# Kernel tuning notes

Hardware: AMD Instinct MI355X
Metric: run time of the kernel (lower is better)

The kernel has to match this reference:

```python
import jax, jax.numpy as jnp
import numpy as np

IN_FEATURES = 512
FEATURES = 512
BATCH, SEQ = 8, 8192


def _ste(x_orig, y_proc):
    return x_orig + jax.lax.stop_gradient(y_proc - x_orig)


def setup_inputs() -> dict:
    key = jax.random.key(0)
    kx, kw = jax.random.split(key)
    x = jax.random.normal(kx, (BATCH, SEQ, IN_FEATURES), dtype=jnp.float32)
    # variance_scaling(1.0, 'fan_in', 'normal'): std = 1/sqrt(fan_in)
    weight = jax.random.normal(kw, (IN_FEATURES, FEATURES), dtype=jnp.float32) / np.sqrt(IN_FEATURES)
    bias = jnp.zeros((FEATURES,), dtype=jnp.float32)
    return {"x": x, "weight": weight, "bias": bias}


def reference(x, weight, bias):
    # BitNet 1.58b-style weight binarization with STE
    weight_centered = weight - jnp.mean(weight)
    weight_bin = jnp.sign(weight_centered)
    weight_bin_ste = _ste(weight, weight_bin)
    scale_gamma = jnp.mean(jnp.abs(weight))
    effective_weight = weight_bin_ste * scale_gamma  # [in, out]
    y = jnp.dot(x, effective_weight) + bias  # [B, S, out]
    # NF4-style activation quant-dequant with STE
    act_clipped = jnp.clip(y, -1.0, 1.0)
    quant_dequant = jnp.round(act_clipped * 7.0) / 7.0
    return _ste(y, quant_dequant)
```

## Files before the change

kernel.cpp:

```cpp
#include <hip/hip_runtime.h>
#include <math.h>

#define K_DIM 512
#define N_DIM 512
#define NLEAF 2048
#define BM 128
#define BN 128
#define BK 32

#define WS_LEAFS 16
#define WS_LEAFA (16 + NLEAF)


__global__ void leaf_kernel(const float* __restrict__ w, float* __restrict__ ws) {
  const int leaf = blockIdx.x * blockDim.x + threadIdx.x;
  const float* p = w + leaf * 128;
  float rs[8], ra[8];
  #pragma unroll
  for (int j = 0; j < 8; ++j) { const float v = p[j]; rs[j] = v; ra[j] = fabsf(v); }
  for (int i = 8; i < 128; i += 8) {
    #pragma unroll
    for (int j = 0; j < 8; ++j) { const float v = p[i + j]; rs[j] += v; ra[j] += fabsf(v); }
  }
  ws[WS_LEAFS + leaf] = ((rs[0] + rs[1]) + (rs[2] + rs[3])) + ((rs[4] + rs[5]) + (rs[6] + rs[7]));
  ws[WS_LEAFA + leaf] = ((ra[0] + ra[1]) + (ra[2] + ra[3])) + ((ra[4] + ra[5]) + (ra[6] + ra[7]));
}

__global__ void tree_kernel(float* __restrict__ ws) {
  __shared__ float bufS[4096];
  __shared__ float bufA[4096];
  const int t = threadIdx.x;
  for (int i = t; i < NLEAF; i += 256) {
    bufS[i] = ws[WS_LEAFS + i];
    bufA[i] = ws[WS_LEAFA + i];
  }
  __syncthreads();
  int src = 0, n = NLEAF;
  while (n > 1) {
    const int dst = src + n;
    n >>= 1;
    for (int i = t; i < n; i += 256) {
      bufS[dst + i] = bufS[src + 2 * i] + bufS[src + 2 * i + 1];
      bufA[dst + i] = bufA[src + 2 * i] + bufA[src + 2 * i + 1];
    }
    __syncthreads();
    src = dst;
  }
  if (t == 0) {
    ws[0] = bufS[src] * (1.0f / 262144.0f);
    ws[1] = bufA[src] * (1.0f / 262144.0f);
  }
}

__global__ __launch_bounds__(256, 4) void gemm_kernel(
    const float* __restrict__ x, const float* __restrict__ w,
    const float* __restrict__ bias, const float* __restrict__ ws,
    float* __restrict__ out) {
  __shared__ float As[BM][BK + 4];
  __shared__ float Bs[BK][BN + 4];

  const float mu = ws[0];
  const float gamma = ws[1];
  const int t = threadIdx.x;
  const int tx = t & 15;
  const int ty = t >> 4;
  const int rowBase = blockIdx.x * BM;
  const int colBase = blockIdx.y * BN;

  float acc[2][2][4][4];
  #pragma unroll
  for (int h = 0; h < 2; ++h)
    #pragma unroll
    for (int g = 0; g < 2; ++g)
      #pragma unroll
      for (int i = 0; i < 4; ++i)
        #pragma unroll
        for (int j = 0; j < 4; ++j) acc[h][g][i][j] = 0.0f;

  for (int kc = 0; kc < K_DIM; kc += BK) {
    #pragma unroll
    for (int p = 0; p < 4; ++p) {
      const int r = (t >> 3) + 32 * p;
      const int k4 = (t & 7) * 4;
      const float4 v = *(const float4*)&x[(size_t)(rowBase + r) * K_DIM + kc + k4];
      *(float4*)&As[r][k4] = v;
    }
    #pragma unroll
    for (int p = 0; p < 4; ++p) {
      const int kk = (t >> 5) + 8 * p;
      const int n4 = (t & 31) * 4;
      const float4 v = *(const float4*)&w[(size_t)(kc + kk) * N_DIM + colBase + n4];
      float4 e;
      const float* vi = &v.x;
      float* ei = &e.x;
      #pragma unroll
      for (int c = 0; c < 4; ++c) {
        const float wv = vi[c];
        const float wc = wv - mu;
        const float bin = (wc > 0.0f) ? 1.0f : ((wc < 0.0f) ? -1.0f : 0.0f);
        const float ste = wv + (bin - wv);
        ei[c] = ste * gamma;
      }
      *(float4*)&Bs[kk][n4] = e;
    }
    __syncthreads();

    #pragma unroll
    for (int kg = 0; kg < 8; ++kg) {
      float4 a0[4], a1[4];
      #pragma unroll
      for (int i = 0; i < 4; ++i) {
        a0[i] = *(const float4*)&As[ty * 4 + i][kg * 4];
        a1[i] = *(const float4*)&As[64 + ty * 4 + i][kg * 4];
      }
      #pragma unroll
      for (int kk = 0; kk < 4; ++kk) {
        const float4 b0 = *(const float4*)&Bs[kg * 4 + kk][tx * 4];
        const float4 b1 = *(const float4*)&Bs[kg * 4 + kk][64 + tx * 4];
        const float* b0p = &b0.x;
        const float* b1p = &b1.x;
        #pragma unroll
        for (int i = 0; i < 4; ++i) {
          const float av0 = (&a0[i].x)[kk];
          const float av1 = (&a1[i].x)[kk];
          #pragma unroll
          for (int j = 0; j < 4; ++j) {
            acc[0][0][i][j] = fmaf(av0, b0p[j], acc[0][0][i][j]);
            acc[0][1][i][j] = fmaf(av0, b1p[j], acc[0][1][i][j]);
            acc[1][0][i][j] = fmaf(av1, b0p[j], acc[1][0][i][j]);
            acc[1][1][i][j] = fmaf(av1, b1p[j], acc[1][1][i][j]);
          }
        }
      }
    }
    __syncthreads();
  }

  #pragma unroll
  for (int h = 0; h < 2; ++h)
    #pragma unroll
    for (int i = 0; i < 4; ++i) {
      const size_t row = (size_t)(rowBase + h * 64 + ty * 4 + i);
      #pragma unroll
      for (int g = 0; g < 2; ++g) {
        const int col = colBase + g * 64 + tx * 4;
        float4 o;
        float* op = &o.x;
        #pragma unroll
        for (int j = 0; j < 4; ++j) {
          const float yb = acc[h][g][i][j] + bias[col + j];
          const float cl = fminf(fmaxf(yb, -1.0f), 1.0f);
          const float t7 = cl * 7.0f;
          const float rr = rintf(t7);
          const float q = rr / 7.0f;
          op[j] = yb + (q - yb);
        }
        *(float4*)&out[row * N_DIM + col] = o;
      }
    }
}

extern "C" void kernel_launch(void* const* d_in, const int* in_sizes, int n_in,
                              void* d_out, int out_size, void* d_ws, size_t ws_size,
                              hipStream_t stream) {
  const float* x = (const float*)d_in[0];
  const float* w = (const float*)d_in[1];
  const float* bias = (const float*)d_in[2];
  float* out = (float*)d_out;
  float* ws = (float*)d_ws;

  const int M = in_sizes[0] / K_DIM;

  leaf_kernel<<<NLEAF / 256, 256, 0, stream>>>(w, ws);
  tree_kernel<<<1, 256, 0, stream>>>(ws);
  gemm_kernel<<<dim3(M / BM, N_DIM / BN), 256, 0, stream>>>(x, w, bias, ws, out);
}
```

Before: 589.4 us.

## Double-buffer shared-memory tiles with register prefetch in GEMM

Converts the GEMM main loop to a double-buffered scheme. The next K-chunk of x and w is loaded into registers before computing on the current shared tile, then written into the alternate buffer, so only one barrier is needed per chunk. BK is halved to 16 to fit two buffers, the As padding is removed, and launch bounds drop to 3 waves per SIMD to allow more registers. The trade-off is more loop iterations with less work each and possible LDS bank conflicts on the unpadded As reads.

```diff
diff --git a/kernel.cpp b/kernel.cpp
--- a/kernel.cpp
+++ b/kernel.cpp
@@ -6,7 +6,8 @@
 #define NLEAF 2048
 #define BM 128
 #define BN 128
-#define BK 32
+#define BK 16
+#define NCHUNK (K_DIM / BK)
 
 #define WS_LEAFS 16
 #define WS_LEAFA (16 + NLEAF)
@@ -52,12 +53,12 @@
   }
 }
 
-__global__ __launch_bounds__(256, 4) void gemm_kernel(
+__global__ __launch_bounds__(256, 3) void gemm_kernel(
     const float* __restrict__ x, const float* __restrict__ w,
     const float* __restrict__ bias, const float* __restrict__ ws,
     float* __restrict__ out) {
-  __shared__ float As[BM][BK + 4];
-  __shared__ float Bs[BK][BN + 4];
+  __shared__ float As[2][BM][BK];
+  __shared__ float Bs[2][BK][BN + 4];
 
   const float mu = ws[0];
   const float gamma = ws[1];
@@ -67,6 +68,16 @@
   const int rowBase = blockIdx.x * BM;
   const int colBase = blockIdx.y * BN;
 
+  const int ar = t >> 2;
+  const int ak4 = (t & 3) * 4;
+  const int bk = t >> 5;
+  const int bn4 = (t & 31) * 4;
+
+  const float* xA0 = x + (size_t)(rowBase + ar) * K_DIM + ak4;
+  const float* xA1 = x + (size_t)(rowBase + ar + 64) * K_DIM + ak4;
+  const float* wB0 = w + (size_t)bk * N_DIM + colBase + bn4;
+  const float* wB1 = w + (size_t)(bk + 8) * N_DIM + colBase + bn4;
+
   float acc[2][2][4][4];
   #pragma unroll
   for (int h = 0; h < 2; ++h)
@@ -77,46 +88,34 @@
         #pragma unroll
         for (int j = 0; j < 4; ++j) acc[h][g][i][j] = 0.0f;
 
-  for (int kc = 0; kc < K_DIM; kc += BK) {
-    #pragma unroll
-    for (int p = 0; p < 4; ++p) {
-      const int r = (t >> 3) + 32 * p;
-      const int k4 = (t & 7) * 4;
-      const float4 v = *(const float4*)&x[(size_t)(rowBase + r) * K_DIM + kc + k4];
-      *(float4*)&As[r][k4] = v;
-    }
-    #pragma unroll
-    for (int p = 0; p < 4; ++p) {
-      const int kk = (t >> 5) + 8 * p;
-      const int n4 = (t & 31) * 4;
-      const float4 v = *(const float4*)&w[(size_t)(kc + kk) * N_DIM + colBase + n4];
-      float4 e;
-      const float* vi = &v.x;
-      float* ei = &e.x;
-      #pragma unroll
-      for (int c = 0; c < 4; ++c) {
-        const float wv = vi[c];
-        const float wc = wv - mu;
-        const float bin = (wc > 0.0f) ? 1.0f : ((wc < 0.0f) ? -1.0f : 0.0f);
-        const float ste = wv + (bin - wv);
-        ei[c] = ste * gamma;
+  auto ste4 = [&](float4 v) -> float4 {
+    float4 e;
+    const float* vi = &v.x;
+    float* ei = &e.x;
+    #pragma unroll
+    for (int c = 0; c < 4; ++c) {
+      const float wv = vi[c];
+      const float wc = wv - mu;
+      const float bin = (wc > 0.0f) ? 1.0f : ((wc < 0.0f) ? -1.0f : 0.0f);
+      const float ste = wv + (bin - wv);
+      ei[c] = ste * gamma;
+    }
+    return e;
+  };
+
+  auto compute = [&](int cur) {
+    #pragma unroll
+    for (int kg = 0; kg < 4; ++kg) {
+      float4 a0[4], a1[4];
+      #pragma unroll
+      for (int i = 0; i < 4; ++i) {
+        a0[i] = *(const float4*)&As[cur][ty * 4 + i][kg * 4];
+        a1[i] = *(const float4*)&As[cur][64 + ty * 4 + i][kg * 4];
       }
-      *(float4*)&Bs[kk][n4] = e;
-    }
-    __syncthreads();
-
-    #pragma unroll
-    for (int kg = 0; kg < 8; ++kg) {
-      float4 a0[4], a1[4];
-      #pragma unroll
-      for (int i = 0; i < 4; ++i) {
-        a0[i] = *(const float4*)&As[ty * 4 + i][kg * 4];
-        a1[i] = *(const float4*)&As[64 + ty * 4 + i][kg * 4];
-      }
       #pragma unroll
       for (int kk = 0; kk < 4; ++kk) {
-        const float4 b0 = *(const float4*)&Bs[kg * 4 + kk][tx * 4];
-        const float4 b1 = *(const float4*)&Bs[kg * 4 + kk][64 + tx * 4];
+        const float4 b0 = *(const float4*)&Bs[cur][kg * 4 + kk][tx * 4];
+        const float4 b1 = *(const float4*)&Bs[cur][kg * 4 + kk][64 + tx * 4];
         const float* b0p = &b0.x;
         const float* b1p = &b1.x;
         #pragma unroll
@@ -133,8 +132,38 @@
         }
       }
     }
+  };
+
+  {
+    const float4 ra0 = *(const float4*)xA0;
+    const float4 ra1 = *(const float4*)xA1;
+    const float4 rb0 = *(const float4*)wB0;
+    const float4 rb1 = *(const float4*)wB1;
+    *(float4*)&As[0][ar][ak4] = ra0;
+    *(float4*)&As[0][ar + 64][ak4] = ra1;
+    *(float4*)&Bs[0][bk][bn4] = ste4(rb0);
+    *(float4*)&Bs[0][bk + 8][bn4] = ste4(rb1);
+  }
+  __syncthreads();
+
+  for (int c = 0; c < NCHUNK - 1; ++c) {
+    const int cur = c & 1;
+    const int kc1 = (c + 1) * BK;
+    const float4 ra0 = *(const float4*)(xA0 + kc1);
+    const float4 ra1 = *(const float4*)(xA1 + kc1);
+    const float4 rb0 = *(const float4*)(wB0 + (size_t)kc1 * N_DIM);
+    const float4 rb1 = *(const float4*)(wB1 + (size_t)kc1 * N_DIM);
+
+    compute(cur);
+
+    const int nxt = cur ^ 1;
+    *(float4*)&As[nxt][ar][ak4] = ra0;
+    *(float4*)&As[nxt][ar + 64][ak4] = ra1;
+    *(float4*)&Bs[nxt][bk][bn4] = ste4(rb0);
+    *(float4*)&Bs[nxt][bk + 8][bn4] = ste4(rb1);
     __syncthreads();
   }
+  compute((NCHUNK - 1) & 1);
 
   #pragma unroll
   for (int h = 0; h < 2; ++h)
```

New measurement: 727.8 us. 1.23x slower.

## Precompute binarized weights and stream them into LDS via global_load_lds

Applied to the files above, without the earlier changes.

Adds a separate kernel that binarizes and scales the weight matrix once into workspace. The GEMM then loads the precomputed effective weights directly into LDS with the async global_load_lds builtin, with no per-tile binarize arithmetic and no register round trip. The B tile drops its padding so the direct copy is contiguous, which may add LDS bank conflicts on the B reads. When the workspace is too small, the code falls back to the old fused kernel.

```diff
diff --git a/kernel.cpp b/kernel.cpp
--- a/kernel.cpp
+++ b/kernel.cpp
@@ -10,6 +10,10 @@
 
 #define WS_LEAFS 16
 #define WS_LEAFA (16 + NLEAF)
+#define WS_EFF 4112
+
+#define GLOBAL_AS __attribute__((address_space(1)))
+#define LDS_AS __attribute__((address_space(3)))
 
 
 __global__ void leaf_kernel(const float* __restrict__ w, float* __restrict__ ws) {
@@ -52,15 +56,31 @@
   }
 }
 
-__global__ __launch_bounds__(256, 4) void gemm_kernel(
-    const float* __restrict__ x, const float* __restrict__ w,
-    const float* __restrict__ bias, const float* __restrict__ ws,
-    float* __restrict__ out) {
-  __shared__ float As[BM][BK + 4];
-  __shared__ float Bs[BK][BN + 4];
-
+__global__ void binarize_kernel(const float* __restrict__ w, float* __restrict__ ws) {
   const float mu = ws[0];
   const float gamma = ws[1];
+  const int i = (blockIdx.x * 256 + threadIdx.x) * 4;
+  const float4 v = *(const float4*)&w[i];
+  float4 e;
+  const float* vi = &v.x;
+  float* ei = &e.x;
+  #pragma unroll
+  for (int c = 0; c < 4; ++c) {
+    const float wv = vi[c];
+    const float wc = wv - mu;
+    const float bin = (wc > 0.0f) ? 1.0f : ((wc < 0.0f) ? -1.0f : 0.0f);
+    const float ste = wv + (bin - wv);
+    ei[c] = ste * gamma;
+  }
+  *(float4*)&ws[WS_EFF + i] = e;
+}
+
+__global__ __launch_bounds__(256, 4) void gemm_kernel_pre(
+    const float* __restrict__ x, const float* __restrict__ eff,
+    const float* __restrict__ bias, float* __restrict__ out) {
+  __shared__ float As[BM][BK + 4];
+  __shared__ float Bs[BK][BN];
+
   const int t = threadIdx.x;
   const int tx = t & 15;
   const int ty = t >> 4;
@@ -80,28 +100,20 @@
   for (int kc = 0; kc < K_DIM; kc += BK) {
     #pragma unroll
     for (int p = 0; p < 4; ++p) {
+      const int off = p * 1024 + t * 4;
+      const int r = off >> 7;
+      const int cdw = off & 127;
+      const float* gsrc = &eff[(size_t)(kc + r) * N_DIM + colBase + cdw];
+      float* ldst = &Bs[0][0] + off;
+      __builtin_amdgcn_global_load_lds((const GLOBAL_AS void*)gsrc,
+                                       (LDS_AS void*)ldst, 16, 0, 0);
+    }
+    #pragma unroll
+    for (int p = 0; p < 4; ++p) {
       const int r = (t >> 3) + 32 * p;
       const int k4 = (t & 7) * 4;
       const float4 v = *(const float4*)&x[(size_t)(rowBase + r) * K_DIM + kc + k4];
       *(float4*)&As[r][k4] = v;
-    }
-    #pragma unroll
-    for (int p = 0; p < 4; ++p) {
-      const int kk = (t >> 5) + 8 * p;
-      const int n4 = (t & 31) * 4;
-      const float4 v = *(const float4*)&w[(size_t)(kc + kk) * N_DIM + colBase + n4];
-      float4 e;
-      const float* vi = &v.x;
-      float* ei = &e.x;
-      #pragma unroll
-      for (int c = 0; c < 4; ++c) {
-        const float wv = vi[c];
-        const float wc = wv - mu;
-        const float bin = (wc > 0.0f) ? 1.0f : ((wc < 0.0f) ? -1.0f : 0.0f);
-        const float ste = wv + (bin - wv);
-        ei[c] = ste * gamma;
-      }
-      *(float4*)&Bs[kk][n4] = e;
     }
     __syncthreads();
 
@@ -160,6 +172,114 @@
     }
 }
 
+__global__ __launch_bounds__(256, 4) void gemm_kernel_fused(
+    const float* __restrict__ x, const float* __restrict__ w,
+    const float* __restrict__ bias, const float* __restrict__ ws,
+    float* __restrict__ out) {
+  __shared__ float As[BM][BK + 4];
+  __shared__ float Bs[BK][BN + 4];
+
+  const float mu = ws[0];
+  const float gamma = ws[1];
+  const int t = threadIdx.x;
+  const int tx = t & 15;
+  const int ty = t >> 4;
+  const int rowBase = blockIdx.x * BM;
+  const int colBase = blockIdx.y * BN;
+
+  float acc[2][2][4][4];
+  #pragma unroll
+  for (int h = 0; h < 2; ++h)
+    #pragma unroll
+    for (int g = 0; g < 2; ++g)
+      #pragma unroll
+      for (int i = 0; i < 4; ++i)
+        #pragma unroll
+        for (int j = 0; j < 4; ++j) acc[h][g][i][j] = 0.0f;
+
+  for (int kc = 0; kc < K_DIM; kc += BK) {
+    #pragma unroll
+    for (int p = 0; p < 4; ++p) {
+      const int r = (t >> 3) + 32 * p;
+      const int k4 = (t & 7) * 4;
+      const float4 v = *(const float4*)&x[(size_t)(rowBase + r) * K_DIM + kc + k4];
+      *(float4*)&As[r][k4] = v;
+    }
+    #pragma unroll
+    for (int p = 0; p < 4; ++p) {
+      const int kk = (t >> 5) + 8 * p;
+      const int n4 = (t & 31) * 4;
+      const float4 v = *(const float4*)&w[(size_t)(kc + kk) * N_DIM + colBase + n4];
+      float4 e;
+      const float* vi = &v.x;
+      float* ei = &e.x;
+      #pragma unroll
+      for (int c = 0; c < 4; ++c) {
+        const float wv = vi[c];
+        const float wc = wv - mu;
+        const float bin = (wc > 0.0f) ? 1.0f : ((wc < 0.0f) ? -1.0f : 0.0f);
+        const float ste = wv + (bin - wv);
+        ei[c] = ste * gamma;
+      }
+      *(float4*)&Bs[kk][n4] = e;
+    }
+    __syncthreads();
+
+    #pragma unroll
+    for (int kg = 0; kg < 8; ++kg) {
+      float4 a0[4], a1[4];
+      #pragma unroll
+      for (int i = 0; i < 4; ++i) {
+        a0[i] = *(const float4*)&As[ty * 4 + i][kg * 4];
+        a1[i] = *(const float4*)&As[64 + ty * 4 + i][kg * 4];
+      }
+      #pragma unroll
+      for (int kk = 0; kk < 4; ++kk) {
+        const float4 b0 = *(const float4*)&Bs[kg * 4 + kk][tx * 4];
+        const float4 b1 = *(const float4*)&Bs[kg * 4 + kk][64 + tx * 4];
+        const float* b0p = &b0.x;
+        const float* b1p = &b1.x;
+        #pragma unroll
+        for (int i = 0; i < 4; ++i) {
+          const float av0 = (&a0[i].x)[kk];
+          const float av1 = (&a1[i].x)[kk];
+          #pragma unroll
+          for (int j = 0; j < 4; ++j) {
+            acc[0][0][i][j] = fmaf(av0, b0p[j], acc[0][0][i][j]);
+            acc[0][1][i][j] = fmaf(av0, b1p[j], acc[0][1][i][j]);
+            acc[1][0][i][j] = fmaf(av1, b0p[j], acc[1][0][i][j]);
+            acc[1][1][i][j] = fmaf(av1, b1p[j], acc[1][1][i][j]);
+          }
+        }
+      }
+    }
+    __syncthreads();
+  }
+
+  #pragma unroll
+  for (int h = 0; h < 2; ++h)
+    #pragma unroll
+    for (int i = 0; i < 4; ++i) {
+      const size_t row = (size_t)(rowBase + h * 64 + ty * 4 + i);
+      #pragma unroll
+      for (int g = 0; g < 2; ++g) {
+        const int col = colBase + g * 64 + tx * 4;
+        float4 o;
+        float* op = &o.x;
+        #pragma unroll
+        for (int j = 0; j < 4; ++j) {
+          const float yb = acc[h][g][i][j] + bias[col + j];
+          const float cl = fminf(fmaxf(yb, -1.0f), 1.0f);
+          const float t7 = cl * 7.0f;
+          const float rr = rintf(t7);
+          const float q = rr / 7.0f;
+          op[j] = yb + (q - yb);
+        }
+        *(float4*)&out[row * N_DIM + col] = o;
+      }
+    }
+}
+
 extern "C" void kernel_launch(void* const* d_in, const int* in_sizes, int n_in,
                               void* d_out, int out_size, void* d_ws, size_t ws_size,
                               hipStream_t stream) {
@@ -173,5 +293,14 @@
 
   leaf_kernel<<<NLEAF / 256, 256, 0, stream>>>(w, ws);
   tree_kernel<<<1, 256, 0, stream>>>(ws);
-  gemm_kernel<<<dim3(M / BM, N_DIM / BN), 256, 0, stream>>>(x, w, bias, ws, out);
-}
+
+  const size_t need = (size_t)(WS_EFF + K_DIM * N_DIM) * sizeof(float);
+  if (ws_size >= need) {
+    binarize_kernel<<<(K_DIM * N_DIM) / (256 * 4), 256, 0, stream>>>(w, ws);
+    gemm_kernel_pre<<<dim3(M / BM, N_DIM / BN), 256, 0, stream>>>(
+        x, ws + WS_EFF, bias, out);
+  } else {
+    gemm_kernel_fused<<<dim3(M / BM, N_DIM / BN), 256, 0, stream>>>(
+        x, w, bias, ws, out);
+  }
+}
```

Result: slower. 615.6 us (+4.4%).
